# Performance work log

Hardware: AMD Instinct MI355X
Metric: run time of the kernel (lower is better)

The kernel has to match this reference:

```python
import jax, jax.numpy as jnp
import numpy as np

SEQ_LEN = 8192
D_MODEL = 1024
D_K = 128
D_V = 128


def setup_inputs() -> dict:
    key = jax.random.key(0)
    kx, kq, kk, kv = jax.random.split(key, 4)
    # xavier-uniform scale for (out, in) linear weights
    def xavier(k, out_f, in_f):
        lim = np.sqrt(6.0 / (in_f + out_f))
        return jax.random.uniform(k, (out_f, in_f), jnp.float32, -lim, lim)
    return {
        "X": jax.random.normal(kx, (SEQ_LEN, D_MODEL), jnp.float32),
        "Wq": xavier(kq, D_K, D_MODEL),
        "Wk": xavier(kk, D_K, D_MODEL),
        "Wv": xavier(kv, D_V, D_MODEL),
    }


def reference(X, Wq, Wk, Wv):
    # X: (S, d_model); W*: (d_k, d_model) torch Linear weights (y = x @ W.T)
    S = X.shape[0]
    Q = X @ Wq.T                      # (S, d_k)
    K = X @ Wk.T                      # (S, d_k)
    V = X @ Wv.T                      # (S, d_v)
    scale = jnp.sqrt(jnp.asarray(D_K, X.dtype))
    scores = (Q @ K.T) / scale        # (S, S)
    causal = jnp.tril(jnp.ones((S, S), bool))
    scores = jnp.where(causal, scores, -jnp.inf)
    weights = jax.nn.softmax(scores, axis=1)
    # dropout p=0.0 -> identity
    Z = weights @ V                   # (S, d_v)
    return Z
```

## Files before the change

### kernel.cpp

```cpp
#include <hip/hip_runtime.h>
#include <hip/hip_bf16.h>

#define S_LEN 8192
#define DM    1024
#define DK    128
#define KSTR  136
#define VSTR  72
#define PSTR2 72
#define SLOTD 1056

typedef __attribute__((ext_vector_type(8))) short bf16x8;
typedef __attribute__((ext_vector_type(8))) _Float16 f16x8;
typedef __attribute__((ext_vector_type(4))) float f32x4;

__device__ __forceinline__ f32x4 mfma16(bf16x8 a, bf16x8 b, f32x4 c) {
    return __builtin_amdgcn_mfma_f32_16x16x32_bf16(a, b, c, 0, 0, 0);
}

__device__ __forceinline__ ushort f2bf(float f) {
    unsigned u = __builtin_bit_cast(unsigned, f);
    u += 0x7FFFu + ((u >> 16) & 1u);
    return (ushort)(u >> 16);
}

__device__ __forceinline__ ushort f2h(float f) {
    return __builtin_bit_cast(ushort, (_Float16)f);
}

__global__ __launch_bounds__(256, 1)
void convert_kernel(const float* __restrict__ X,
                    const float* __restrict__ Wq,
                    const float* __restrict__ Wk,
                    const float* __restrict__ Wv,
                    _Float16* __restrict__ Xh,
                    _Float16* __restrict__ Wh) {
    const int NX4 = S_LEN * DM / 4;
    const int NW4 = DK * DM / 4;
    const int total4 = NX4 + 3 * NW4;
    for (int i = blockIdx.x * 256 + threadIdx.x; i < total4; i += gridDim.x * 256) {
        const float4* src;
        _Float16* dst;
        int off;
        if (i < NX4) {
            src = (const float4*)X; dst = Xh; off = i;
        } else {
            const int w = i - NX4;
            const int which = w / NW4;
            off = w - which * NW4;
            src = (const float4*)(which == 0 ? Wq : (which == 1 ? Wk : Wv));
            dst = Wh + which * (DK * DM);
        }
        const float4 v = src[off];
        union { _Float16 h[4]; uint2 u; } p;
        p.h[0] = (_Float16)v.x; p.h[1] = (_Float16)v.y;
        p.h[2] = (_Float16)v.z; p.h[3] = (_Float16)v.w;
        *(uint2*)(dst + (size_t)off * 4) = p.u;
    }
}

__global__ __launch_bounds__(256)
void proj_gemm_kernel(const _Float16* __restrict__ Xh,
                      const _Float16* __restrict__ Wh,
                      ushort* __restrict__ Qb,
                      ushort* __restrict__ Kb,
                      ushort* __restrict__ Vtb) {
    __shared__ _Float16 Ash[32 * 32];
    __shared__ _Float16 Bsh[128 * 32];

    const int tid  = threadIdx.x;
    const int lane = tid & 63;
    const int quad = lane >> 4;
    const int l15  = lane & 15;
    const int wv   = tid >> 6;
    const int wm   = wv & 1;
    const int wn   = wv >> 1;
    const int m0   = blockIdx.x * 32;
    const int nb   = blockIdx.y;
    const _Float16* Wbase = Wh + nb * (DK * DM);

    f32x4 acc[4];
#pragma unroll
    for (int ni = 0; ni < 4; ++ni) acc[ni] = (f32x4){0.f, 0.f, 0.f, 0.f};

    for (int kk = 0; kk < DM; kk += 32) {
        __syncthreads();
        for (int s = tid; s < 640; s += 256) {
            if (s < 128) {
                const int row = s >> 2, sg = s & 3;
                __builtin_amdgcn_global_load_lds(
                    (const __attribute__((address_space(1))) void*)(Xh + (size_t)(m0 + row) * DM + kk + sg * 8),
                    (__attribute__((address_space(3))) void*)(Ash + s * 8), 16, 0, 0);
            } else {
                const int t = s - 128;
                const int row = t >> 2, sg = t & 3;
                __builtin_amdgcn_global_load_lds(
                    (const __attribute__((address_space(1))) void*)(Wbase + (size_t)row * DM + kk + sg * 8),
                    (__attribute__((address_space(3))) void*)(Bsh + t * 8), 16, 0, 0);
            }
        }
        __syncthreads();

        const f16x8 af = *(const f16x8*)(Ash + (wm * 16 + l15) * 32 + quad * 8);
        f16x8 bf[4];
#pragma unroll
        for (int t = 0; t < 4; ++t)
            bf[t] = *(const f16x8*)(Bsh + (wn * 64 + t * 16 + l15) * 32 + quad * 8);
#pragma unroll
        for (int ni = 0; ni < 4; ++ni)
            acc[ni] = __builtin_amdgcn_mfma_f32_16x16x32_f16(af, bf[ni], acc[ni], 0, 0, 0);
    }

    if (nb == 2) {
#pragma unroll
        for (int ni = 0; ni < 4; ++ni) {
            const int n = wn * 64 + ni * 16 + l15;
            const int m = m0 + wm * 16 + quad * 4;
            union { ushort h[4]; uint2 u; } p;
#pragma unroll
            for (int r = 0; r < 4; ++r) p.h[r] = f2bf(acc[ni][r]);
            *(uint2*)(Vtb + (size_t)n * S_LEN + m) = p.u;
        }
    } else {
        ushort* Ob = (nb == 0) ? Qb : Kb;
        const float sc = (nb == 0) ? 0.088388347648318447f * 1.4426950408889634f : 1.0f;
#pragma unroll
        for (int ni = 0; ni < 4; ++ni) {
            const int n = wn * 64 + ni * 16 + l15;
#pragma unroll
            for (int r = 0; r < 4; ++r) {
                const int m = m0 + wm * 16 + quad * 4 + r;
                Ob[(size_t)m * DK + n] = f2bf(acc[ni][r] * sc);
            }
        }
    }
}

__global__ __launch_bounds__(256, 3)
void flash_partial_kernel(const ushort* __restrict__ Qg,
                          const ushort* __restrict__ Kg,
                          const ushort* __restrict__ Vtg,
                          float* __restrict__ Part) {
    __shared__ __align__(16) ushort Ks [64 * KSTR];
    __shared__ __align__(16) ushort Vts[128 * VSTR];
    __shared__ __align__(16) ushort PlA[4 * 16 * PSTR2];

    const int b = 575 - (int)blockIdx.x;
    int g = 0;
    while (b >= 8 * (g + 1) * (g + 2)) ++g;
    const int idx   = b - 8 * g * (g + 1);
    const int qb    = 16 * g + idx / (g + 1);
    const int chunk = idx % (g + 1);
    const int nkt   = qb + 1;
    const int kt_lo = chunk * nkt / (g + 1);
    const int kt_hi = (chunk + 1) * nkt / (g + 1);

    const int tid  = threadIdx.x;
    const int wv   = tid >> 6;
    const int lane = tid & 63;
    const int quad = lane >> 4;
    const int l15  = lane & 15;
    const int q0w  = qb * 64 + wv * 16;
    ushort* Pl = PlA + wv * 16 * PSTR2;

    bf16x8 qf[4];
    {
        const ushort* qrow = Qg + (size_t)(q0w + l15) * DK + quad * 8;
#pragma unroll
        for (int kc = 0; kc < 4; ++kc) qf[kc] = *(const bf16x8*)(qrow + kc * 32);
    }

    const bf16x8 ones = {(short)0x3F80, (short)0x3F80, (short)0x3F80, (short)0x3F80,
                         (short)0x3F80, (short)0x3F80, (short)0x3F80, (short)0x3F80};

    float m_[4], l_[4];
#pragma unroll
    for (int r = 0; r < 4; ++r) { m_[r] = -__builtin_inff(); l_[r] = 0.f; }
    f32x4 acc[8];
#pragma unroll
    for (int d = 0; d < 8; ++d) acc[d] = (f32x4){0.f, 0.f, 0.f, 0.f};

    bf16x8 stg[8];
#define LOAD_TILE(K0)                                                          \
    {                                                                          \
        const int k0_ = (K0);                                                  \
        _Pragma("unroll")                                                      \
        for (int i = 0; i < 8; ++i) {                                          \
            const int c = tid + (i << 8);                                      \
            if (c < 1024) {                                                    \
                const int row = c >> 4, ch = c & 15;                           \
                stg[i] = *(const bf16x8*)(Kg + (size_t)(k0_ + row) * DK + ch * 8); \
            } else {                                                           \
                const int cc = c - 1024;                                       \
                const int row = cc >> 3, ch = cc & 7;                          \
                stg[i] = *(const bf16x8*)(Vtg + (size_t)row * S_LEN + k0_ + ch * 8); \
            }                                                                  \
        }                                                                      \
    }

    LOAD_TILE(kt_lo * 64)

    for (int kt = kt_lo; kt < kt_hi; ++kt) {
        const int k0 = kt * 64;

        __syncthreads();
#pragma unroll
        for (int i = 0; i < 8; ++i) {
            const int c = tid + (i << 8);
            if (c < 1024) {
                const int row = c >> 4, ch = c & 15;
                *(bf16x8*)(Ks + row * KSTR + ch * 8) = stg[i];
            } else {
                const int cc = c - 1024;
                const int row = cc >> 3, ch = cc & 7;
                *(bf16x8*)(Vts + row * VSTR + ch * 8) = stg[i];
            }
        }
        if (kt + 1 < kt_hi) LOAD_TILE((kt + 1) * 64)
        __syncthreads();

        f32x4 Sr[4];
#pragma unroll
        for (int nb = 0; nb < 4; ++nb) {
            Sr[nb] = (f32x4){0.f, 0.f, 0.f, 0.f};
            const ushort* kb = Ks + (nb * 16 + l15) * KSTR + quad * 8;
#pragma unroll
            for (int kc = 0; kc < 4; ++kc)
                Sr[nb] = mfma16(qf[kc], *(const bf16x8*)(kb + kc * 32), Sr[nb]);
        }

        if (k0 + 63 > q0w) {
#pragma unroll
            for (int nb = 0; nb < 4; ++nb) {
                const int kg = k0 + nb * 16 + l15;
#pragma unroll
                for (int r = 0; r < 4; ++r)
                    if (kg > q0w + quad * 4 + r) Sr[nb][r] = -__builtin_inff();
            }
        }

        float al[4];
#pragma unroll
        for (int r = 0; r < 4; ++r) {
            float v = m_[r];
#pragma unroll
            for (int nb = 0; nb < 4; ++nb) v = fmaxf(v, Sr[nb][r]);
            v = fmaxf(v, __shfl_xor(v, 1));
            v = fmaxf(v, __shfl_xor(v, 2));
            v = fmaxf(v, __shfl_xor(v, 4));
            v = fmaxf(v, __shfl_xor(v, 8));
            al[r] = exp2f(m_[r] - v);
            m_[r] = v;
        }
#pragma unroll
        for (int nb = 0; nb < 4; ++nb) {
#pragma unroll
            for (int r = 0; r < 4; ++r) {
                const float p = exp2f(Sr[nb][r] - m_[r]);
                Pl[(quad * 4 + r) * PSTR2 + nb * 16 + l15] = f2bf(p);
            }
        }
#pragma unroll
        for (int d = 0; d < 8; ++d)
#pragma unroll
            for (int r = 0; r < 4; ++r) acc[d][r] *= al[r];

        f32x4 sacc = (f32x4){0.f, 0.f, 0.f, 0.f};
#pragma unroll
        for (int kcp = 0; kcp < 2; ++kcp) {
            const bf16x8 pf = *(const bf16x8*)(Pl + l15 * PSTR2 + kcp * 32 + quad * 8);
            sacc = mfma16(pf, ones, sacc);
#pragma unroll
            for (int db = 0; db < 8; ++db) {
                const bf16x8 vf = *(const bf16x8*)(Vts + (db * 16 + l15) * VSTR + kcp * 32 + quad * 8);
                acc[db] = mfma16(pf, vf, acc[db]);
            }
        }
#pragma unroll
        for (int r = 0; r < 4; ++r) l_[r] = l_[r] * al[r] + sacc[r];
    }
#undef LOAD_TILE

    const int qt16 = qb * 4 + wv;
    float* slot = Part + (size_t)(qt16 * 8 + chunk) * SLOTD;
    if (l15 == 0) {
#pragma unroll
        for (int r = 0; r < 4; ++r) {
            slot[quad * 4 + r]      = m_[r];
            slot[16 + quad * 4 + r] = l_[r];
        }
    }
    uint* slotO = (uint*)(slot + 32);
#pragma unroll
    for (int d = 0; d < 8; ++d)
#pragma unroll
        for (int r = 0; r < 4; ++r) {
            const float v  = acc[d][r];
            const float vp = __shfl_xor(v, 1);
            if ((l15 & 1) == 0) {
                const int row = quad * 4 + r;
                const uint u = (uint)f2h(v) | ((uint)f2h(vp) << 16);
                slotO[(row * 128 + d * 16 + l15) >> 1] = u;
            }
        }
}

__global__ __launch_bounds__(256)
void flash_merge_kernel(const float* __restrict__ Part, float* __restrict__ Out) {
    __shared__ float Ms[16], Ls[16];
    __shared__ float Sc[8][16];
    const int qt = blockIdx.x;
    const int q0 = qt * 16;
    const int P  = (qt >> 6) + 1;
    const int tid = threadIdx.x;
    const float* base = Part + (size_t)qt * 8 * SLOTD;

    if (tid < 16) {
        float M = -__builtin_inff();
        for (int p = 0; p < P; ++p) M = fmaxf(M, base[p * SLOTD + tid]);
        float L = 0.f;
        for (int p = 0; p < P; ++p)
            L += base[p * SLOTD + 16 + tid] * exp2f(base[p * SLOTD + tid] - M);
        Ms[tid] = M; Ls[tid] = L;
    }
    __syncthreads();
    if (tid < 128) {
        const int p = tid >> 4, row = tid & 15;
        Sc[p][row] = (p < P) ? exp2f(base[p * SLOTD + row] - Ms[row]) : 0.f;
    }
    __syncthreads();

#pragma unroll
    for (int j = tid; j < 1024; j += 256) {
        const int row = j >> 6, c2 = j & 63;
        float o0 = 0.f, o1 = 0.f;
        for (int p = 0; p < P; ++p) {
            const uint u = ((const uint*)(base + p * SLOTD + 32))[row * 64 + c2];
            const float sc = Sc[p][row];
            o0 += (float)__builtin_bit_cast(_Float16, (ushort)(u & 0xFFFF)) * sc;
            o1 += (float)__builtin_bit_cast(_Float16, (ushort)(u >> 16)) * sc;
        }
        const float inv = 1.0f / Ls[row];
        float2 o; o.x = o0 * inv; o.y = o1 * inv;
        *(float2*)(Out + (size_t)(q0 + row) * DK + c2 * 2) = o;
    }
}

extern "C" void kernel_launch(void* const* d_in, const int* in_sizes, int n_in,
                              void* d_out, int out_size, void* d_ws, size_t ws_size,
                              hipStream_t stream) {
    const float* X  = (const float*)d_in[0];
    const float* Wq = (const float*)d_in[1];
    const float* Wk = (const float*)d_in[2];
    const float* Wv = (const float*)d_in[3];
    ushort* ws  = (ushort*)d_ws;
    ushort* Qb  = ws;
    ushort* Kb  = ws + (size_t)S_LEN * DK;
    ushort* Vtb = ws + 2 * (size_t)S_LEN * DK;
    _Float16* Xh = (_Float16*)(ws + 3 * (size_t)S_LEN * DK);
    _Float16* Wh = Xh + (size_t)S_LEN * DM;
    float* Part = (float*)Xh;
    float* Out = (float*)d_out;

    convert_kernel<<<1024, 256, 0, stream>>>(X, Wq, Wk, Wv, Xh, Wh);
    proj_gemm_kernel<<<dim3(256, 3), 256, 0, stream>>>(Xh, Wh, Qb, Kb, Vtb);
    flash_partial_kernel<<<576, 256, 0, stream>>>(Qb, Kb, Vtb, Part);
    flash_merge_kernel<<<512, 256, 0, stream>>>(Part, Out);
}
```

Measured before the change: 178.4 us.

## Keep softmax probabilities in registers, add lazy rescale and finer split-K grid

The flash kernel now computes S transposed (K as the A operand). Each lane then holds one query's scores, so the probabilities can be packed straight into the PV MFMA operand with v_cvt_pk_bf16 instead of going through an LDS round trip. Row max and sum reductions become two cross-quad shuffles, and the ones-MFMA row-sum is dropped. The accumulator rescale is skipped unless the max grows by more than 8, and V is stored with a permuted layout to match. The work split changes to up to 8 chunks per query block over 996 blocks, and s_setprio is added around the MFMA phases; the extra blocks raise parallelism but also partial-merge traffic.

```diff
diff --git a/kernel.cpp b/kernel.cpp
--- a/kernel.cpp
+++ b/kernel.cpp
@@ -6,7 +6,6 @@
 #define DK    128
 #define KSTR  136
 #define VSTR  72
-#define PSTR2 72
 #define SLOTD 1056
 
 typedef __attribute__((ext_vector_type(8))) short bf16x8;
@@ -25,6 +24,12 @@
 
 __device__ __forceinline__ ushort f2h(float f) {
     return __builtin_bit_cast(ushort, (_Float16)f);
+}
+
+__device__ __forceinline__ uint cvt_pk_bf16(float a, float b) {
+    uint r;
+    asm("v_cvt_pk_bf16_f32 %0, %1, %2" : "=v"(r) : "v"(a), "v"(b));
+    return r;
 }
 
 __global__ __launch_bounds__(256, 1)
@@ -142,17 +147,21 @@
                           float* __restrict__ Part) {
     __shared__ __align__(16) ushort Ks [64 * KSTR];
     __shared__ __align__(16) ushort Vts[128 * VSTR];
-    __shared__ __align__(16) ushort PlA[4 * 16 * PSTR2];
-
-    const int b = 575 - (int)blockIdx.x;
-    int g = 0;
-    while (b >= 8 * (g + 1) * (g + 2)) ++g;
-    const int idx   = b - 8 * g * (g + 1);
-    const int qb    = 16 * g + idx / (g + 1);
-    const int chunk = idx % (g + 1);
+
+    const int b = 995 - (int)blockIdx.x;
+    int qb, chunk;
+    if (b < 36) {
+        int q = 0;
+        while (b >= (q + 1) * (q + 2) / 2) ++q;
+        qb = q; chunk = b - q * (q + 1) / 2;
+    } else {
+        qb = 8 + ((b - 36) >> 3);
+        chunk = (b - 36) & 7;
+    }
     const int nkt   = qb + 1;
-    const int kt_lo = chunk * nkt / (g + 1);
-    const int kt_hi = (chunk + 1) * nkt / (g + 1);
+    const int NC    = nkt < 8 ? nkt : 8;
+    const int kt_lo = chunk * nkt / NC;
+    const int kt_hi = (chunk + 1) * nkt / NC;
 
     const int tid  = threadIdx.x;
     const int wv   = tid >> 6;
@@ -160,7 +169,6 @@
     const int quad = lane >> 4;
     const int l15  = lane & 15;
     const int q0w  = qb * 64 + wv * 16;
-    ushort* Pl = PlA + wv * 16 * PSTR2;
 
     bf16x8 qf[4];
     {
@@ -169,12 +177,8 @@
         for (int kc = 0; kc < 4; ++kc) qf[kc] = *(const bf16x8*)(qrow + kc * 32);
     }
 
-    const bf16x8 ones = {(short)0x3F80, (short)0x3F80, (short)0x3F80, (short)0x3F80,
-                         (short)0x3F80, (short)0x3F80, (short)0x3F80, (short)0x3F80};
-
-    float m_[4], l_[4];
-#pragma unroll
-    for (int r = 0; r < 4; ++r) { m_[r] = -__builtin_inff(); l_[r] = 0.f; }
+    float m_ = -__builtin_inff();
+    float l_ = 0.f;
     f32x4 acc[8];
 #pragma unroll
     for (int d = 0; d < 8; ++d) acc[d] = (f32x4){0.f, 0.f, 0.f, 0.f};
@@ -212,82 +216,101 @@
             } else {
                 const int cc = c - 1024;
                 const int row = cc >> 3, ch = cc & 7;
-                *(bf16x8*)(Vts + row * VSTR + ch * 8) = stg[i];
+                const int s_lo = ((ch >> 2) << 5) + ((ch & 1) << 4) + (((ch >> 1) & 1) << 2);
+                union { bf16x8 v; uint2 q2[2]; } u;
+                u.v = stg[i];
+                ushort* vb = Vts + row * VSTR + s_lo;
+                *(uint2*)vb       = u.q2[0];
+                *(uint2*)(vb + 8) = u.q2[1];
             }
         }
         if (kt + 1 < kt_hi) LOAD_TILE((kt + 1) * 64)
         __syncthreads();
 
         f32x4 Sr[4];
+        __builtin_amdgcn_s_setprio(1);
 #pragma unroll
         for (int nb = 0; nb < 4; ++nb) {
             Sr[nb] = (f32x4){0.f, 0.f, 0.f, 0.f};
             const ushort* kb = Ks + (nb * 16 + l15) * KSTR + quad * 8;
 #pragma unroll
             for (int kc = 0; kc < 4; ++kc)
-                Sr[nb] = mfma16(qf[kc], *(const bf16x8*)(kb + kc * 32), Sr[nb]);
-        }
+                Sr[nb] = mfma16(*(const bf16x8*)(kb + kc * 32), qf[kc], Sr[nb]);
+        }
+        __builtin_amdgcn_s_setprio(0);
 
         if (k0 + 63 > q0w) {
+            const int qg = q0w + l15;
 #pragma unroll
             for (int nb = 0; nb < 4; ++nb) {
-                const int kg = k0 + nb * 16 + l15;
+                const int kg = k0 + nb * 16 + quad * 4;
 #pragma unroll
                 for (int r = 0; r < 4; ++r)
-                    if (kg > q0w + quad * 4 + r) Sr[nb][r] = -__builtin_inff();
-            }
-        }
-
-        float al[4];
-#pragma unroll
-        for (int r = 0; r < 4; ++r) {
-            float v = m_[r];
-#pragma unroll
-            for (int nb = 0; nb < 4; ++nb) v = fmaxf(v, Sr[nb][r]);
-            v = fmaxf(v, __shfl_xor(v, 1));
-            v = fmaxf(v, __shfl_xor(v, 2));
-            v = fmaxf(v, __shfl_xor(v, 4));
-            v = fmaxf(v, __shfl_xor(v, 8));
-            al[r] = exp2f(m_[r] - v);
-            m_[r] = v;
-        }
-#pragma unroll
-        for (int nb = 0; nb < 4; ++nb) {
+                    if (kg + r > qg) Sr[nb][r] = -__builtin_inff();
+            }
+        }
+
+        float pmax;
+        {
+            float a0 = fmaxf(fmaxf(Sr[0][0], Sr[0][1]), fmaxf(Sr[0][2], Sr[0][3]));
+            float a1 = fmaxf(fmaxf(Sr[1][0], Sr[1][1]), fmaxf(Sr[1][2], Sr[1][3]));
+            float a2 = fmaxf(fmaxf(Sr[2][0], Sr[2][1]), fmaxf(Sr[2][2], Sr[2][3]));
+            float a3 = fmaxf(fmaxf(Sr[3][0], Sr[3][1]), fmaxf(Sr[3][2], Sr[3][3]));
+            pmax = fmaxf(fmaxf(a0, a1), fmaxf(a2, a3));
+            pmax = fmaxf(pmax, __shfl_xor(pmax, 16));
+            pmax = fmaxf(pmax, __shfl_xor(pmax, 32));
+        }
+        if (__any(pmax > m_ + 8.f)) {
+            const float mnew = fmaxf(m_, pmax);
+            const float al = __builtin_amdgcn_exp2f(m_ - mnew);
+            m_ = mnew;
+            l_ *= al;
+            float alr[4];
+#pragma unroll
+            for (int r = 0; r < 4; ++r)
+                alr[r] = __shfl(al, (lane & 48) | (((lane >> 4) & 3) * 4 + r));
+#pragma unroll
+            for (int d = 0; d < 8; ++d)
+#pragma unroll
+                for (int r = 0; r < 4; ++r) acc[d][r] *= alr[r];
+        }
+
+        float p[4][4];
+        float rs = 0.f;
+#pragma unroll
+        for (int nb = 0; nb < 4; ++nb)
 #pragma unroll
             for (int r = 0; r < 4; ++r) {
-                const float p = exp2f(Sr[nb][r] - m_[r]);
-                Pl[(quad * 4 + r) * PSTR2 + nb * 16 + l15] = f2bf(p);
-            }
-        }
-#pragma unroll
-        for (int d = 0; d < 8; ++d)
-#pragma unroll
-            for (int r = 0; r < 4; ++r) acc[d][r] *= al[r];
-
-        f32x4 sacc = (f32x4){0.f, 0.f, 0.f, 0.f};
+                p[nb][r] = __builtin_amdgcn_exp2f(Sr[nb][r] - m_);
+                rs += p[nb][r];
+            }
+        rs += __shfl_xor(rs, 16);
+        rs += __shfl_xor(rs, 32);
+        l_ += rs;
+
+        __builtin_amdgcn_s_setprio(1);
 #pragma unroll
         for (int kcp = 0; kcp < 2; ++kcp) {
-            const bf16x8 pf = *(const bf16x8*)(Pl + l15 * PSTR2 + kcp * 32 + quad * 8);
-            sacc = mfma16(pf, ones, sacc);
+            union { uint u[4]; bf16x8 v; } pf;
+            pf.u[0] = cvt_pk_bf16(p[2 * kcp][0],     p[2 * kcp][1]);
+            pf.u[1] = cvt_pk_bf16(p[2 * kcp][2],     p[2 * kcp][3]);
+            pf.u[2] = cvt_pk_bf16(p[2 * kcp + 1][0], p[2 * kcp + 1][1]);
+            pf.u[3] = cvt_pk_bf16(p[2 * kcp + 1][2], p[2 * kcp + 1][3]);
 #pragma unroll
             for (int db = 0; db < 8; ++db) {
                 const bf16x8 vf = *(const bf16x8*)(Vts + (db * 16 + l15) * VSTR + kcp * 32 + quad * 8);
-                acc[db] = mfma16(pf, vf, acc[db]);
-            }
-        }
-#pragma unroll
-        for (int r = 0; r < 4; ++r) l_[r] = l_[r] * al[r] + sacc[r];
+                acc[db] = mfma16(pf.v, vf, acc[db]);
+            }
+        }
+        __builtin_amdgcn_s_setprio(0);
     }
 #undef LOAD_TILE
 
     const int qt16 = qb * 4 + wv;
     float* slot = Part + (size_t)(qt16 * 8 + chunk) * SLOTD;
-    if (l15 == 0) {
-#pragma unroll
-        for (int r = 0; r < 4; ++r) {
-            slot[quad * 4 + r]      = m_[r];
-            slot[16 + quad * 4 + r] = l_[r];
-        }
+    if (quad == 0) {
+        slot[l15]      = m_;
+        slot[16 + l15] = l_;
     }
     uint* slotO = (uint*)(slot + 32);
 #pragma unroll
@@ -310,7 +333,8 @@
     __shared__ float Sc[8][16];
     const int qt = blockIdx.x;
     const int q0 = qt * 16;
-    const int P  = (qt >> 6) + 1;
+    const int qb = qt >> 2;
+    const int P  = (qb + 1 < 8) ? (qb + 1) : 8;
     const int tid = threadIdx.x;
     const float* base = Part + (size_t)qt * 8 * SLOTD;
 
@@ -363,6 +387,6 @@
 
     convert_kernel<<<1024, 256, 0, stream>>>(X, Wq, Wk, Wv, Xh, Wh);
     proj_gemm_kernel<<<dim3(256, 3), 256, 0, stream>>>(Xh, Wh, Qb, Kb, Vtb);
-    flash_partial_kernel<<<576, 256, 0, stream>>>(Qb, Kb, Vtb, Part);
+    flash_partial_kernel<<<996, 256, 0, stream>>>(Qb, Kb, Vtb, Part);
     flash_merge_kernel<<<512, 256, 0, stream>>>(Part, Out);
 }
```

After: 158.3 us. -11.2%, faster.
